# Optimization experiments

Hardware: AMD Instinct MI355X
Metric: run time of the kernel (lower is better)

The kernel has to match this reference:

```python
import jax, jax.numpy as jnp
import numpy as np

EPS = 1e-6
D = 1152          # hidden_size
NH_HEADS = 16     # num_attention_heads
HD = D // NH_HEADS
INTER = 4304      # intermediate_size
H4 = 4 * D        # 4608
I4 = 4 * INTER    # 17216
B, H, W = 8, 64, 64
WH, WW = 2, 2


def setup_inputs() -> dict:
    key = jax.random.key(0)
    ks = jax.random.split(key, 12)
    s = 0.02
    inp = {
        "hidden_states": jax.random.normal(ks[0], (B, H * W, D), jnp.float32),
        "tgt_sizes": jnp.full((B, 2), 64, dtype=jnp.int32),
        "attention_mask": jnp.zeros((B, 1, 1, H * W), jnp.float32),
        "ln1_g": jnp.ones((D,), jnp.float32),
        "ln1_b": jnp.zeros((D,), jnp.float32),
        "qkv_w": jax.random.normal(ks[1], (D, 3 * D), jnp.float32) * s,
        "qkv_b": jnp.zeros((3 * D,), jnp.float32),
        "out_w": jax.random.normal(ks[2], (D, D), jnp.float32) * s,
        "out_b": jnp.zeros((D,), jnp.float32),
        "pre_g": jnp.ones((H4,), jnp.float32),
        "pre_b": jnp.zeros((H4,), jnp.float32),
        "w1": jax.random.normal(ks[3], (H4, I4), jnp.float32) * s,
        "b1": jnp.zeros((I4,), jnp.float32),
        "w2": jax.random.normal(ks[4], (I4, D), jnp.float32) * s,
        "b2": jnp.zeros((D,), jnp.float32),
    }
    return inp


def _layernorm(x, g, b):
    m = x.mean(-1, keepdims=True)
    v = ((x - m) ** 2).mean(-1, keepdims=True)
    return (x - m) * jax.lax.rsqrt(v + EPS) * g + b


def _partition(x):
    # x: [B, H*W, D] -> windows [B, nh*nw, wh*ww, D]
    nh, nw = H // WH, W // WW
    x = x.reshape(B, nh, WH, nw, WW, D)
    x = x.transpose(0, 1, 3, 2, 4, 5)  # [B, nh, nw, wh, ww, D]
    return x.reshape(B, nh * nw, WH * WW, D)


def _unpartition(x):
    # windows [B, nh*nw, wh*ww, D] -> [B, H*W, D]
    nh, nw = H // WH, W // WW
    x = x.reshape(B, nh, nw, WH, WW, D)
    x = x.transpose(0, 1, 3, 2, 4, 5)  # [B, nh, wh, nw, ww, D]
    return x.reshape(B, H * W, D)


def reference(hidden_states, tgt_sizes, attention_mask, ln1_g, ln1_b,
              qkv_w, qkv_b, out_w, out_b, pre_g, pre_b, w1, b1, w2, b2):
    nh, nw = H // WH, W // WW
    nwin = nh * nw
    residual = hidden_states
    hs = _layernorm(hidden_states, ln1_g, ln1_b)

    # window self-attention over 4-token windows
    xw = _partition(hs).reshape(B * nwin, WH * WW, D)
    qkv = xw @ qkv_w + qkv_b                               # [N, 4, 3D]
    q, k, v = jnp.split(qkv, 3, axis=-1)
    q = q.reshape(-1, WH * WW, NH_HEADS, HD)
    k = k.reshape(-1, WH * WW, NH_HEADS, HD)
    v = v.reshape(-1, WH * WW, NH_HEADS, HD)
    scale = HD ** -0.5
    scores = jnp.einsum('nqhd,nkhd->nhqk', q, k) * scale
    probs = jax.nn.softmax(scores, axis=-1)
    o = jnp.einsum('nhqk,nkhd->nqhd', probs, v).reshape(-1, WH * WW, D)
    o = o @ out_w + out_b
    attn_out = _unpartition(o.reshape(B, nwin, WH * WW, D))
    hs = residual + attn_out                               # [B, H*W, D]

    # MLP downsample over 2x2 windows
    xw = _partition(hs)                                    # [B, nwin, 4, D]
    res = xw.mean(axis=2)                                  # [B, nwin, D]
    xf = xw.reshape(B, nwin, WH * WW * D)                  # [B, nwin, 4D]
    xf = _layernorm(xf, pre_g, pre_b)
    xf = jax.nn.gelu(xf @ w1 + b1, approximate=True)
    xf = xf @ w2 + b2
    new_hidden = xf + res                                  # [B, nwin, D]

    new_tgt_sizes = tgt_sizes // 2
    # all samples fully valid -> mask of zeros (no -inf positions)
    min_val = jnp.finfo(new_hidden.dtype).min
    valid = jnp.arange(nwin)[None, :] < (new_tgt_sizes[:, 0] * new_tgt_sizes[:, 1])[:, None]
    new_attention_mask = ((~valid).astype(new_hidden.dtype) * min_val)[:, None, None, :]
    return new_hidden, new_tgt_sizes, new_attention_mask
```

## Files before the change

kernel.cpp:

```cpp
#include <hip/hip_runtime.h>
#include <cstdint>
#include <cstddef>

#define DEV __device__ __forceinline__
typedef unsigned short u16;
typedef unsigned int u32;
typedef short bf16x8 __attribute__((ext_vector_type(8)));
typedef float f32x4 __attribute__((ext_vector_type(4)));

typedef __attribute__((address_space(1))) u32 GU32;
typedef __attribute__((address_space(3))) u32 LU32;

DEV float bf2f(u16 v){ u32 x = ((u32)v)<<16; float f; __builtin_memcpy(&f,&x,4); return f; }
DEV u16 f2bf(float f){ u32 x; __builtin_memcpy(&x,&f,4); return (u16)((x + 0x7fffu + ((x>>16)&1u)) >> 16); }

DEV int map_row(int r){
  int b = r>>12, rr = r&4095;
  int win = rr>>2, t = rr&3;
  int wy = win>>5, wx = win&31;
  int y = (wy<<1) + (t>>1), x = (wx<<1) + (t&1);
  return (b<<12) + (y<<6) + x;
}

DEV void gl_lds16(const void* g, void* l){
  __builtin_amdgcn_global_load_lds((const GU32*)g, (LU32*)l, 16, 0, 0);
}

DEV void block_red2(float& s, float& ss, float* red){
  #pragma unroll
  for (int o=32;o;o>>=1){ s += __shfl_down(s,o); ss += __shfl_down(ss,o); }
  const int wv = threadIdx.x>>6;
  if ((threadIdx.x&63)==0){ red[wv*2]=s; red[wv*2+1]=ss; }
  __syncthreads();
  s  = red[0]+red[2]+red[4]+red[6];
  ss = red[1]+red[3]+red[5]+red[7];
}

__launch_bounds__(256)
__global__ void tconv_k(const float* __restrict__ W, u16* __restrict__ WT, int K, int N){
  __shared__ float tl[64][65];
  const int n0 = blockIdx.x << 6, k0 = blockIdx.y << 6;
  const int tx = threadIdx.x & 63, ty = threadIdx.x >> 6;
  #pragma unroll
  for (int rr = 0; rr < 64; rr += 4)
    tl[rr+ty][tx] = W[(size_t)(k0+rr+ty)*N + (n0+tx)];
  __syncthreads();
  #pragma unroll
  for (int rr = 0; rr < 64; rr += 4)
    WT[(size_t)(n0+rr+ty)*K + (k0+tx)] = f2bf(tl[tx][rr+ty]);
}

__launch_bounds__(256)
__global__ void ln1_k(const float* __restrict__ X, const float* __restrict__ g,
                      const float* __restrict__ b, u16* __restrict__ Y){
  __shared__ float red[8];
  const int r = blockIdx.x;
  const float* xr = X + (size_t)map_row(r)*1152;
  const int tid = threadIdx.x;
  const bool has2 = tid < 32;
  float4 v0 = ((const float4*)xr)[tid];
  float4 v1 = {0,0,0,0};
  float s  = v0.x+v0.y+v0.z+v0.w;
  float ss = v0.x*v0.x+v0.y*v0.y+v0.z*v0.z+v0.w*v0.w;
  if (has2){
    v1 = ((const float4*)xr)[tid+256];
    s  += v1.x+v1.y+v1.z+v1.w;
    ss += v1.x*v1.x+v1.y*v1.y+v1.z*v1.z+v1.w*v1.w;
  }
  block_red2(s, ss, red);
  const float mean = s*(1.0f/1152.0f);
  const float rstd = rsqrtf(ss*(1.0f/1152.0f) - mean*mean + 1e-6f);
  u16* yr = Y + (size_t)r*1152;
  {
    float4 gg = ((const float4*)g)[tid];
    float4 bb = ((const float4*)b)[tid];
    ushort4 o;
    o.x = f2bf((v0.x-mean)*rstd*gg.x + bb.x);
    o.y = f2bf((v0.y-mean)*rstd*gg.y + bb.y);
    o.z = f2bf((v0.z-mean)*rstd*gg.z + bb.z);
    o.w = f2bf((v0.w-mean)*rstd*gg.w + bb.w);
    *(ushort4*)(yr + tid*4) = o;
  }
  if (has2){
    float4 gg = ((const float4*)g)[tid+256];
    float4 bb = ((const float4*)b)[tid+256];
    ushort4 o;
    o.x = f2bf((v1.x-mean)*rstd*gg.x + bb.x);
    o.y = f2bf((v1.y-mean)*rstd*gg.y + bb.y);
    o.z = f2bf((v1.z-mean)*rstd*gg.z + bb.z);
    o.w = f2bf((v1.w-mean)*rstd*gg.w + bb.w);
    *(ushort4*)(yr + (tid+256)*4) = o;
  }
}

#define BAR()  asm volatile("s_barrier" ::: "memory")
#define LGKM0() do{ asm volatile("s_waitcnt lgkmcnt(0)" ::: "memory"); \
                    __builtin_amdgcn_sched_barrier(0); }while(0)
#define VMW8() asm volatile("s_waitcnt vmcnt(8)" ::: "memory")
#define VMW6() asm volatile("s_waitcnt vmcnt(6)" ::: "memory")
#define VMW4() asm volatile("s_waitcnt vmcnt(4)" ::: "memory")
#define VMW0() asm volatile("s_waitcnt vmcnt(0)" ::: "memory")
#define WNONE() do{}while(0)

template<int EPI>
__launch_bounds__(512, 1)
__global__ void gemm8p_k(const u16* __restrict__ A, const u16* __restrict__ BT,
                         int M, int N, int K, int lda, int ldb,
                         void* __restrict__ C, int ldc,
                         const float* __restrict__ bias,
                         const float* __restrict__ aux,
                         int nTM, int nTN)
{
  __shared__ __align__(16) u16 LS[2][2][2][8192];
  const int tid = threadIdx.x;
  const int lane = tid & 63;
  const int wave = tid >> 6;
  const int wr = wave >> 2, wc = wave & 3;

  const int bid  = blockIdx.x;
  const int band = 16 * nTN;
  const int bb   = bid / band, rr_ = bid % band;
  int mcnt = nTM - (bb<<4); if (mcnt > 16) mcnt = 16;
  const int mt = (bb<<4) + rr_ % mcnt;
  const int nt = rr_ / mcnt;
  const int m0 = mt << 8, n0 = nt << 8;

  const int lr1 = tid >> 3, sl = tid & 7;
  const int x_  = sl ^ (lr1 & 7);
  const int grow = ((x_ >> 2) << 7) + lr1;
  const int q_   = x_ & 3;
  const u16* aS = A  + (size_t)(m0 + grow)*lda + q_*8;
  const u16* bS = BT + (size_t)(n0 + grow)*ldb + q_*8;
  const size_t aR64 = (size_t)64*lda, bR64 = (size_t)64*ldb;

  const int l15 = lane & 15, l7 = lane & 7, qh = lane >> 4;
  const int aOff = l15*64 + ((((wr<<2)|qh) ^ l7) << 3);
  const int bOff = ((wc&1)<<12) + l15*64 + (((((wc>>1)<<2)|qh) ^ l7) << 3);

  f32x4 acc[8][4] = {};
  bf16x8 af[4], bv[4];
  const int NT = K >> 6;

#define ST(op_, db_, kh_, t_) do{ \
    const u16* src__ = (op_ ? bS : aS) + (size_t)(t_)*64 + (kh_)*32; \
    u16* dst__ = &LS[(db_)][(op_)][(kh_)][tid*8]; \
    gl_lds16(src__, dst__); \
    gl_lds16(src__ + (op_ ? bR64 : aR64), dst__ + 4096); \
  }while(0)

#define READA(base_, mh_) do{ \
    const u16* ap__ = (base_) + aOff + ((mh_)?4096:0); \
    _Pragma("unroll") for (int i__=0;i__<4;i__++) af[i__] = *(const bf16x8*)(ap__ + i__*1024); \
  }while(0)

#define READB(base_) do{ \
    const u16* bp__ = (base_) + bOff; \
    _Pragma("unroll") for (int i__=0;i__<4;i__++) bv[i__] = *(const bf16x8*)(bp__ + i__*1024); \
  }while(0)

#define MFMA16(B_) do{ \
    __builtin_amdgcn_s_setprio(1); \
    _Pragma("unroll") for (int i__=0;i__<4;i__++) \
      _Pragma("unroll") for (int n__=0;n__<4;n__++) \
        acc[(B_)+i__][n__] = __builtin_amdgcn_mfma_f32_16x16x32_bf16(af[i__], bv[n__], acc[(B_)+i__][n__], 0,0,0); \
    __builtin_amdgcn_s_setprio(0); \
  }while(0)

#define GROUP(t_, SE12, SE3, Wp1, Wp3) do{ \
    const int cb__ = (t_) & 1; \
    const u16* rA0__ = &LS[cb__][0][0][0]; \
    const u16* rB0__ = &LS[cb__][1][0][0]; \
    const u16* rA1__ = &LS[cb__][0][1][0]; \
    const u16* rB1__ = &LS[cb__][1][1][0]; \
    READB(rB0__); READA(rA0__, 0); \
    BAR(); LGKM0(); MFMA16(0); \
    READA(rA0__, 1); if (SE12) ST(0, cb__^1, 1, (t_)+1); \
    Wp1(); BAR(); LGKM0(); MFMA16(4); \
    READB(rB1__); READA(rA1__, 0); if (SE12) ST(1, cb__^1, 1, (t_)+1); \
    BAR(); LGKM0(); MFMA16(0); \
    READA(rA1__, 1); if (SE3) { ST(0, cb__, 0, (t_)+2); ST(1, cb__, 0, (t_)+2); } \
    Wp3(); BAR(); LGKM0(); MFMA16(4); \
  }while(0)

  ST(0,0,0,0); ST(1,0,0,0); ST(0,0,1,0); ST(1,0,1,0); ST(0,1,0,1); ST(1,1,0,1);
  VMW8(); BAR();

  int t = 0;
  for (; t < NT-2; ++t) GROUP(t, 1, 1, VMW6, VMW8);
  GROUP(t, 1, 0, VMW6, VMW4); ++t;
  GROUP(t, 0, 0, VMW0, WNONE);

#undef GROUP
#undef MFMA16
#undef READB
#undef READA
#undef ST

  #pragma unroll
  for (int mi=0;mi<8;mi++){
    const int row = m0 + (wr<<7) + (mi<<4) + ((lane>>4)<<2);
    #pragma unroll
    for (int ni=0;ni<4;ni++){
      const int col = n0 + (wc<<6) + (ni<<4) + (lane&15);
      if (col < N){
        const float bvv = bias[col];
        #pragma unroll
        for (int r2=0;r2<4;r2++){
          const int rw = row + r2;
          float v = acc[mi][ni][r2] + bvv;
          if (EPI==0){
            ((u16*)C)[(size_t)rw*ldc + col] = f2bf(v);
          } else if (EPI==1){
            v += aux[(size_t)map_row(rw)*ldc + col];
            ((u16*)C)[(size_t)rw*ldc + col] = f2bf(v);
          } else if (EPI==2){
            const float x = v;
            const float c = 0.7978845608028654f*(x + 0.044715f*x*x*x);
            v = 0.5f*x*(1.0f + tanhf(c));
            ((u16*)C)[(size_t)rw*ldc + col] = f2bf(v);
          } else {
            v += aux[(size_t)rw*ldc + col];
            ((float*)C)[(size_t)rw*ldc + col] = v;
          }
        }
      }
    }
  }
}

__launch_bounds__(256)
__global__ void attn_k(const u16* __restrict__ QKV, u16* __restrict__ O){
  const int wave = threadIdx.x >> 6, lane = threadIdx.x & 63;
  const int wg = blockIdx.x*4 + wave;
  const int t = lane >> 4, h = lane & 15;
  const u16* base = QKV + (size_t)wg*4*3456;

  float q[72];
  {
    const u16* qp = base + t*3456 + h*72;
    #pragma unroll
    for (int i=0;i<9;i++){
      bf16x8 v = *(const bf16x8*)(qp + i*8);
      #pragma unroll
      for (int j=0;j<8;j++) q[i*8+j] = bf2f((u16)v[j]);
    }
  }
  float sc[4];
  #pragma unroll
  for (int tp=0;tp<4;tp++){
    const u16* kp = base + tp*3456 + 1152 + h*72;
    float a = 0.f;
    #pragma unroll
    for (int i=0;i<9;i++){
      bf16x8 v = *(const bf16x8*)(kp + i*8);
      #pragma unroll
      for (int j=0;j<8;j++) a += q[i*8+j]*bf2f((u16)v[j]);
    }
    sc[tp] = a * 0.11785113019775793f;
  }
  const float mx = fmaxf(fmaxf(sc[0],sc[1]), fmaxf(sc[2],sc[3]));
  float p[4]; float sum = 0.f;
  #pragma unroll
  for (int tp=0;tp<4;tp++){ p[tp] = __expf(sc[tp]-mx); sum += p[tp]; }
  const float inv = 1.0f/sum;
  float o[72];
  #pragma unroll
  for (int i=0;i<72;i++) o[i] = 0.f;
  #pragma unroll
  for (int tp=0;tp<4;tp++){
    const float w = p[tp]*inv;
    const u16* vp = base + tp*3456 + 2304 + h*72;
    #pragma unroll
    for (int i=0;i<9;i++){
      bf16x8 v = *(const bf16x8*)(vp + i*8);
      #pragma unroll
      for (int j=0;j<8;j++) o[i*8+j] += w*bf2f((u16)v[j]);
    }
  }
  u16* op = O + (size_t)(wg*4+t)*1152 + h*72;
  #pragma unroll
  for (int i=0;i<9;i++){
    bf16x8 sv;
    #pragma unroll
    for (int j=0;j<8;j++) sv[j] = (short)f2bf(o[i*8+j]);
    *(bf16x8*)(op + i*8) = sv;
  }
}

__launch_bounds__(256)
__global__ void ln2res_k(const u16* __restrict__ hs2, const float* __restrict__ g,
                         const float* __restrict__ b, u16* __restrict__ Y,
                         float* __restrict__ res){
  __shared__ float buf[4608];
  __shared__ float red[8];
  const int w = blockIdx.x;
  const u16* xr = hs2 + (size_t)w*4608;
  float s = 0.f, ss = 0.f;
  for (int i = threadIdx.x*8; i < 4608; i += 2048){
    bf16x8 v = *(const bf16x8*)(xr + i);
    #pragma unroll
    for (int j=0;j<8;j++){
      float f = bf2f((u16)v[j]);
      buf[i+j] = f; s += f; ss += f*f;
    }
  }
  block_red2(s, ss, red);
  const float mean = s*(1.0f/4608.0f);
  const float rstd = rsqrtf(ss*(1.0f/4608.0f) - mean*mean + 1e-6f);
  u16* yr = Y + (size_t)w*4608;
  for (int i = threadIdx.x*8; i < 4608; i += 2048){
    bf16x8 sv;
    #pragma unroll
    for (int j=0;j<8;j++)
      sv[j] = (short)f2bf((buf[i+j]-mean)*rstd*g[i+j] + b[i+j]);
    *(bf16x8*)(yr + i) = sv;
  }
  for (int d = threadIdx.x; d < 1152; d += 256)
    res[(size_t)w*1152 + d] = 0.25f*(buf[d]+buf[d+1152]+buf[d+2304]+buf[d+3456]);
}

__global__ void tail_k(const int* __restrict__ tgt, float* __restrict__ out){
  const int tid = blockIdx.x*blockDim.x + threadIdx.x;
  float* t_out = out + 9437184;
  float* m_out = t_out + 16;
  if (tid < 16) t_out[tid] = (float)(tgt[tid] / 2);
  for (int i = tid; i < 8192; i += 256*32){
    const int b = i >> 10, w = i & 1023;
    const int lim = (tgt[b*2]/2) * (tgt[b*2+1]/2);
    m_out[i] = (w < lim) ? 0.0f : -3.40282346638528859812e+38f;
  }
}

extern "C" void kernel_launch(void* const* d_in, const int* in_sizes, int n_in,
                              void* d_out, int out_size, void* d_ws, size_t ws_size,
                              hipStream_t stream){
  const float* hidden = (const float*)d_in[0];
  const int*   tgt    = (const int*)  d_in[1];
  const float* ln1_g  = (const float*)d_in[3];
  const float* ln1_b  = (const float*)d_in[4];
  const float* qkv_w  = (const float*)d_in[5];
  const float* qkv_b  = (const float*)d_in[6];
  const float* out_w  = (const float*)d_in[7];
  const float* out_b  = (const float*)d_in[8];
  const float* pre_g  = (const float*)d_in[9];
  const float* pre_b  = (const float*)d_in[10];
  const float* w1     = (const float*)d_in[11];
  const float* b1     = (const float*)d_in[12];
  const float* w2     = (const float*)d_in[13];
  const float* b2     = (const float*)d_in[14];
  float* out = (float*)d_out;

  char* p = (char*)d_ws;
  auto alloc = [&](size_t bytes)->void*{ void* r = p; p += (bytes + 255) & ~(size_t)255; return r; };
  u16* w1T = (u16*)alloc(17216ull*4608*2);
  u16* w2T = (u16*)alloc(1152ull*17216*2);
  u16* wqT = (u16*)alloc(3456ull*1152*2);
  u16* woT = (u16*)alloc(1152ull*1152*2);
  u16* Xln = (u16*)alloc(32768ull*1152*2);
  char* qr = (char*)alloc(32768ull*3456*2);
  u16*   QKV  = (u16*)qr;
  u16*   hs2  = (u16*)qr;
  float* res  = (float*)(qr + 75497472);
  u16*   xfln = (u16*)(qr + 150994944);
  size_t fixed = (size_t)(p - (char*)d_ws);
  size_t avail = ws_size > fixed ? ws_size - fixed : 0;
  long long crl = (long long)((avail / (17216ull*2)) & ~(size_t)255);
  int CR = (int)(crl > 8192 ? 8192 : crl);
  if (CR < 256) CR = 256;
  u16* h1 = (u16*)p;

  tconv_k<<<dim3(17216/64, 4608/64), 256, 0, stream>>>(w1, w1T, 4608, 17216);
  tconv_k<<<dim3(1152/64, 17216/64), 256, 0, stream>>>(w2, w2T, 17216, 1152);
  tconv_k<<<dim3(3456/64, 1152/64), 256, 0, stream>>>(qkv_w, wqT, 1152, 3456);
  tconv_k<<<dim3(1152/64, 1152/64), 256, 0, stream>>>(out_w, woT, 1152, 1152);
  ln1_k<<<32768, 256, 0, stream>>>(hidden, ln1_g, ln1_b, Xln);
  gemm8p_k<0><<<dim3(128*14), 512, 0, stream>>>(Xln, wqT, 32768, 3456, 1152, 1152, 1152,
                                                QKV, 3456, qkv_b, nullptr, 128, 14);
  attn_k<<<2048, 256, 0, stream>>>(QKV, Xln);
  gemm8p_k<1><<<dim3(128*5), 512, 0, stream>>>(Xln, woT, 32768, 1152, 1152, 1152, 1152,
                                               hs2, 1152, out_b, hidden, 128, 5);
  ln2res_k<<<8192, 256, 0, stream>>>(hs2, pre_g, pre_b, xfln, res);
  for (int r0 = 0; r0 < 8192; r0 += CR){
    const int m = (8192 - r0 < CR) ? (8192 - r0) : CR;
    gemm8p_k<2><<<dim3((m>>8)*68), 512, 0, stream>>>(xfln + (size_t)r0*4608, w1T,
                                                     m, 17216, 4608, 4608, 4608,
                                                     h1, 17216, b1, nullptr, m>>8, 68);
    gemm8p_k<3><<<dim3((m>>8)*5), 512, 0, stream>>>(h1, w2T,
                                                    m, 1152, 17216, 17216, 17216,
                                                    out + (size_t)r0*1152, 1152, b2,
                                                    res + (size_t)r0*1152, m>>8, 5);
  }
  tail_k<<<32, 256, 0, stream>>>(tgt, out);
}
```

Measured before the change: 2.411 ms.

## Load GEMM B operand directly from global into registers, stage only A in LDS

The GEMM kernel drops LDS staging for the weight (B) operand. Each wave now loads its B fragments straight from global memory into registers, while A is still double-buffered in LDS. The main loop is simplified to one barrier per K-tile, replacing the four-phase grouped schedule with its fine-grained waitcnts. This halves LDS traffic and footprint and cuts barriers, but B reads become uncoalesced 16-byte per-lane global loads with no cross-wave reuse, and the direct loads may expose global latency.

```diff
diff --git a/kernel.cpp b/kernel.cpp
--- a/kernel.cpp
+++ b/kernel.cpp
@@ -94,24 +94,18 @@
 }
 
 #define BAR()  asm volatile("s_barrier" ::: "memory")
-#define LGKM0() do{ asm volatile("s_waitcnt lgkmcnt(0)" ::: "memory"); \
-                    __builtin_amdgcn_sched_barrier(0); }while(0)
 #define VMW8() asm volatile("s_waitcnt vmcnt(8)" ::: "memory")
-#define VMW6() asm volatile("s_waitcnt vmcnt(6)" ::: "memory")
-#define VMW4() asm volatile("s_waitcnt vmcnt(4)" ::: "memory")
-#define VMW0() asm volatile("s_waitcnt vmcnt(0)" ::: "memory")
-#define WNONE() do{}while(0)
 
 template<int EPI>
 __launch_bounds__(512, 1)
-__global__ void gemm8p_k(const u16* __restrict__ A, const u16* __restrict__ BT,
+__global__ void gemmbr_k(const u16* __restrict__ A, const u16* __restrict__ BT,
                          int M, int N, int K, int lda, int ldb,
                          void* __restrict__ C, int ldc,
                          const float* __restrict__ bias,
                          const float* __restrict__ aux,
                          int nTM, int nTN)
 {
-  __shared__ __align__(16) u16 LS[2][2][2][8192];
+  __shared__ __align__(16) u16 LSA[2][2][8192];
   const int tid = threadIdx.x;
   const int lane = tid & 63;
   const int wave = tid >> 6;
@@ -129,72 +123,75 @@
   const int x_  = sl ^ (lr1 & 7);
   const int grow = ((x_ >> 2) << 7) + lr1;
   const int q_   = x_ & 3;
-  const u16* aS = A  + (size_t)(m0 + grow)*lda + q_*8;
-  const u16* bS = BT + (size_t)(n0 + grow)*ldb + q_*8;
-  const size_t aR64 = (size_t)64*lda, bR64 = (size_t)64*ldb;
+  const u16* aS = A + (size_t)(m0 + grow)*lda + q_*8;
+  const size_t aR64 = (size_t)64*lda;
 
   const int l15 = lane & 15, l7 = lane & 7, qh = lane >> 4;
   const int aOff = l15*64 + ((((wr<<2)|qh) ^ l7) << 3);
-  const int bOff = ((wc&1)<<12) + l15*64 + (((((wc>>1)<<2)|qh) ^ l7) << 3);
+
+  const u16* bP[4];
+  #pragma unroll
+  for (int ni=0;ni<4;ni++)
+    bP[ni] = BT + (size_t)(n0 + (wc<<6) + (ni<<4) + l15)*ldb + (qh<<3);
 
   f32x4 acc[8][4] = {};
-  bf16x8 af[4], bv[4];
+  bf16x8 af[8];
+  bf16x8 bB[4][2];
   const int NT = K >> 6;
 
-#define ST(op_, db_, kh_, t_) do{ \
-    const u16* src__ = (op_ ? bS : aS) + (size_t)(t_)*64 + (kh_)*32; \
-    u16* dst__ = &LS[(db_)][(op_)][(kh_)][tid*8]; \
-    gl_lds16(src__, dst__); \
-    gl_lds16(src__ + (op_ ? bR64 : aR64), dst__ + 4096); \
+#define STAGEA(slotW_, t_) do{ \
+    _Pragma("unroll") for (int kh__=0;kh__<2;kh__++){ \
+      const u16* src__ = aS + (size_t)(t_)*64 + kh__*32; \
+      u16* dst__ = (slotW_) + kh__*8192 + tid*8; \
+      gl_lds16(src__, dst__); \
+      gl_lds16(src__ + aR64, dst__ + 4096); \
+    } \
   }while(0)
 
-#define READA(base_, mh_) do{ \
-    const u16* ap__ = (base_) + aOff + ((mh_)?4096:0); \
-    _Pragma("unroll") for (int i__=0;i__<4;i__++) af[i__] = *(const bf16x8*)(ap__ + i__*1024); \
+#define DSA(slotR_, kh_) do{ \
+    const u16* ap__ = (slotR_) + (kh_)*8192 + aOff; \
+    _Pragma("unroll") for (int j__=0;j__<8;j__++) af[j__] = *(const bf16x8*)(ap__ + j__*1024); \
   }while(0)
 
-#define READB(base_) do{ \
-    const u16* bp__ = (base_) + bOff; \
-    _Pragma("unroll") for (int i__=0;i__<4;i__++) bv[i__] = *(const bf16x8*)(bp__ + i__*1024); \
+#define LOADB(t_) do{ \
+    _Pragma("unroll") for (int ni__=0;ni__<4;ni__++) \
+      _Pragma("unroll") for (int h__=0;h__<2;h__++) \
+        bB[ni__][h__] = *(const bf16x8*)(bP[ni__] + (size_t)(t_)*64 + h__*32); \
   }while(0)
 
-#define MFMA16(B_) do{ \
+#define MFMAH(h_) do{ \
     __builtin_amdgcn_s_setprio(1); \
-    _Pragma("unroll") for (int i__=0;i__<4;i__++) \
-      _Pragma("unroll") for (int n__=0;n__<4;n__++) \
-        acc[(B_)+i__][n__] = __builtin_amdgcn_mfma_f32_16x16x32_bf16(af[i__], bv[n__], acc[(B_)+i__][n__], 0,0,0); \
+    _Pragma("unroll") for (int mi__=0;mi__<8;mi__++) \
+      _Pragma("unroll") for (int ni__=0;ni__<4;ni__++) \
+        acc[mi__][ni__] = __builtin_amdgcn_mfma_f32_16x16x32_bf16(af[mi__], bB[ni__][h_], acc[mi__][ni__], 0,0,0); \
     __builtin_amdgcn_s_setprio(0); \
   }while(0)
 
-#define GROUP(t_, SE12, SE3, Wp1, Wp3) do{ \
-    const int cb__ = (t_) & 1; \
-    const u16* rA0__ = &LS[cb__][0][0][0]; \
-    const u16* rB0__ = &LS[cb__][1][0][0]; \
-    const u16* rA1__ = &LS[cb__][0][1][0]; \
-    const u16* rB1__ = &LS[cb__][1][1][0]; \
-    READB(rB0__); READA(rA0__, 0); \
-    BAR(); LGKM0(); MFMA16(0); \
-    READA(rA0__, 1); if (SE12) ST(0, cb__^1, 1, (t_)+1); \
-    Wp1(); BAR(); LGKM0(); MFMA16(4); \
-    READB(rB1__); READA(rA1__, 0); if (SE12) ST(1, cb__^1, 1, (t_)+1); \
-    BAR(); LGKM0(); MFMA16(0); \
-    READA(rA1__, 1); if (SE3) { ST(0, cb__, 0, (t_)+2); ST(1, cb__, 0, (t_)+2); } \
-    Wp3(); BAR(); LGKM0(); MFMA16(4); \
-  }while(0)
-
-  ST(0,0,0,0); ST(1,0,0,0); ST(0,0,1,0); ST(1,0,1,0); ST(0,1,0,1); ST(1,1,0,1);
+  STAGEA(&LSA[0][0][0], 0);
+  __builtin_amdgcn_sched_barrier(0);
+  LOADB(0);
   VMW8(); BAR();
 
-  int t = 0;
-  for (; t < NT-2; ++t) GROUP(t, 1, 1, VMW6, VMW8);
-  GROUP(t, 1, 0, VMW6, VMW4); ++t;
-  GROUP(t, 0, 0, VMW0, WNONE);
-
-#undef GROUP
-#undef MFMA16
-#undef READB
-#undef READA
-#undef ST
+  for (int t = 0; t < NT; ++t){
+    u16* slotR = &LSA[t&1][0][0];
+    u16* slotW = &LSA[(t+1)&1][0][0];
+    const bool SA = (t+1 < NT);
+    if (SA){ STAGEA(slotW, t+1); __builtin_amdgcn_sched_barrier(0); }
+    DSA(slotR, 0);
+    MFMAH(0);
+    DSA(slotR, 1);
+    MFMAH(1);
+    if (SA){
+      LOADB(t+1);
+      VMW8();
+      BAR();
+    }
+  }
+
+#undef MFMAH
+#undef LOADB
+#undef DSA
+#undef STAGEA
 
   #pragma unroll
   for (int mi=0;mi<8;mi++){
@@ -374,18 +371,18 @@
   tconv_k<<<dim3(3456/64, 1152/64), 256, 0, stream>>>(qkv_w, wqT, 1152, 3456);
   tconv_k<<<dim3(1152/64, 1152/64), 256, 0, stream>>>(out_w, woT, 1152, 1152);
   ln1_k<<<32768, 256, 0, stream>>>(hidden, ln1_g, ln1_b, Xln);
-  gemm8p_k<0><<<dim3(128*14), 512, 0, stream>>>(Xln, wqT, 32768, 3456, 1152, 1152, 1152,
+  gemmbr_k<0><<<dim3(128*14), 512, 0, stream>>>(Xln, wqT, 32768, 3456, 1152, 1152, 1152,
                                                 QKV, 3456, qkv_b, nullptr, 128, 14);
   attn_k<<<2048, 256, 0, stream>>>(QKV, Xln);
-  gemm8p_k<1><<<dim3(128*5), 512, 0, stream>>>(Xln, woT, 32768, 1152, 1152, 1152, 1152,
+  gemmbr_k<1><<<dim3(128*5), 512, 0, stream>>>(Xln, woT, 32768, 1152, 1152, 1152, 1152,
                                                hs2, 1152, out_b, hidden, 128, 5);
   ln2res_k<<<8192, 256, 0, stream>>>(hs2, pre_g, pre_b, xfln, res);
   for (int r0 = 0; r0 < 8192; r0 += CR){
     const int m = (8192 - r0 < CR) ? (8192 - r0) : CR;
-    gemm8p_k<2><<<dim3((m>>8)*68), 512, 0, stream>>>(xfln + (size_t)r0*4608, w1T,
+    gemmbr_k<2><<<dim3((m>>8)*68), 512, 0, stream>>>(xfln + (size_t)r0*4608, w1T,
                                                      m, 17216, 4608, 4608, 4608,
                                                      h1, 17216, b1, nullptr, m>>8, 68);
-    gemm8p_k<3><<<dim3((m>>8)*5), 512, 0, stream>>>(h1, w2T,
+    gemmbr_k<3><<<dim3((m>>8)*5), 512, 0, stream>>>(h1, w2T,
                                                     m, 1152, 17216, 17216, 17216,
                                                     out + (size_t)r0*1152, 1152, b2,
                                                     res + (size_t)r0*1152, m>>8, 5);
```

After: 3.698 ms, median of 2. +53.4%, slower.

## Split-K the down-projection GEMM and reduce partials in a finalize kernel

Applied to the files above, without the earlier changes.

Adds a K-split mode to the GEMM kernel, driven by blockIdx.y and a per-split tile count. Each split writes fp32 partial sums to a scratch buffer that reuses the xfln workspace. The second MLP GEMM now runs as two K-halves, which doubles the block count from 160 tiles. A new fin_k kernel then sums the two partials with the bias and residual. The intent is better CU occupancy for a GEMM whose output tile grid is small, at the cost of extra fp32 partial traffic and one more kernel launch. The path is used only when the workspace fits the full 8192-row chunk.

```diff
diff --git a/kernel.cpp b/kernel.cpp
--- a/kernel.cpp
+++ b/kernel.cpp
@@ -109,13 +109,17 @@
                          void* __restrict__ C, int ldc,
                          const float* __restrict__ bias,
                          const float* __restrict__ aux,
-                         int nTM, int nTN)
+                         int nTM, int nTN, int ktile0)
 {
   __shared__ __align__(16) u16 LS[2][2][2][8192];
   const int tid = threadIdx.x;
   const int lane = tid & 63;
   const int wave = tid >> 6;
   const int wr = wave >> 2, wc = wave & 3;
+
+  const int ky  = (int)blockIdx.y;
+  const int kt0 = ky * ktile0;
+  const int NT  = (ky == (int)gridDim.y - 1) ? (K>>6) - kt0 : ktile0;
 
   const int bid  = blockIdx.x;
   const int band = 16 * nTN;
@@ -129,8 +133,8 @@
   const int x_  = sl ^ (lr1 & 7);
   const int grow = ((x_ >> 2) << 7) + lr1;
   const int q_   = x_ & 3;
-  const u16* aS = A  + (size_t)(m0 + grow)*lda + q_*8;
-  const u16* bS = BT + (size_t)(n0 + grow)*ldb + q_*8;
+  const u16* aS = A  + (size_t)(m0 + grow)*lda + (size_t)kt0*64 + q_*8;
+  const u16* bS = BT + (size_t)(n0 + grow)*ldb + (size_t)kt0*64 + q_*8;
   const size_t aR64 = (size_t)64*lda, bR64 = (size_t)64*ldb;
 
   const int l15 = lane & 15, l7 = lane & 7, qh = lane >> 4;
@@ -139,7 +143,6 @@
 
   f32x4 acc[8][4] = {};
   bf16x8 af[4], bv[4];
-  const int NT = K >> 6;
 
 #define ST(op_, db_, kh_, t_) do{ \
     const u16* src__ = (op_ ? bS : aS) + (size_t)(t_)*64 + (kh_)*32; \
@@ -196,6 +199,8 @@
 #undef READA
 #undef ST
 
+  float* Cp = (EPI==4) ? ((float*)C + (size_t)ky*M*ldc) : nullptr;
+
   #pragma unroll
   for (int mi=0;mi<8;mi++){
     const int row = m0 + (wr<<7) + (mi<<4) + ((lane>>4)<<2);
@@ -203,7 +208,7 @@
     for (int ni=0;ni<4;ni++){
       const int col = n0 + (wc<<6) + (ni<<4) + (lane&15);
       if (col < N){
-        const float bvv = bias[col];
+        const float bvv = (EPI==4) ? 0.f : bias[col];
         #pragma unroll
         for (int r2=0;r2<4;r2++){
           const int rw = row + r2;
@@ -218,13 +223,34 @@
             const float c = 0.7978845608028654f*(x + 0.044715f*x*x*x);
             v = 0.5f*x*(1.0f + tanhf(c));
             ((u16*)C)[(size_t)rw*ldc + col] = f2bf(v);
-          } else {
+          } else if (EPI==3){
             v += aux[(size_t)rw*ldc + col];
             ((float*)C)[(size_t)rw*ldc + col] = v;
+          } else {
+            Cp[(size_t)rw*ldc + col] = v;
           }
         }
       }
     }
+  }
+}
+
+__launch_bounds__(256)
+__global__ void fin_k(const float* __restrict__ P, const float* __restrict__ res,
+                      const float* __restrict__ bias, float* __restrict__ out){
+  const int total4 = 8192*288;
+  for (int i = blockIdx.x*256 + threadIdx.x; i < total4; i += 2048*256){
+    const int c4 = i % 288;
+    float4 a = ((const float4*)P)[i];
+    float4 b = ((const float4*)P)[i + total4];
+    float4 r = ((const float4*)res)[i];
+    float4 g = ((const float4*)bias)[c4];
+    float4 o;
+    o.x = a.x + b.x + r.x + g.x;
+    o.y = a.y + b.y + r.y + g.y;
+    o.z = a.z + b.z + r.z + g.z;
+    o.w = a.w + b.w + r.w + g.w;
+    ((float4*)out)[i] = o;
   }
 }
 
@@ -362,6 +388,7 @@
   u16*   hs2  = (u16*)qr;
   float* res  = (float*)(qr + 75497472);
   u16*   xfln = (u16*)(qr + 150994944);
+  float* P    = (float*)(qr + 150994944);
   size_t fixed = (size_t)(p - (char*)d_ws);
   size_t avail = ws_size > fixed ? ws_size - fixed : 0;
   long long crl = (long long)((avail / (17216ull*2)) & ~(size_t)255);
@@ -375,20 +402,28 @@
   tconv_k<<<dim3(1152/64, 1152/64), 256, 0, stream>>>(out_w, woT, 1152, 1152);
   ln1_k<<<32768, 256, 0, stream>>>(hidden, ln1_g, ln1_b, Xln);
   gemm8p_k<0><<<dim3(128*14), 512, 0, stream>>>(Xln, wqT, 32768, 3456, 1152, 1152, 1152,
-                                                QKV, 3456, qkv_b, nullptr, 128, 14);
+                                                QKV, 3456, qkv_b, nullptr, 128, 14, 1152>>6);
   attn_k<<<2048, 256, 0, stream>>>(QKV, Xln);
   gemm8p_k<1><<<dim3(128*5), 512, 0, stream>>>(Xln, woT, 32768, 1152, 1152, 1152, 1152,
-                                               hs2, 1152, out_b, hidden, 128, 5);
+                                               hs2, 1152, out_b, hidden, 128, 5, 1152>>6);
   ln2res_k<<<8192, 256, 0, stream>>>(hs2, pre_g, pre_b, xfln, res);
-  for (int r0 = 0; r0 < 8192; r0 += CR){
-    const int m = (8192 - r0 < CR) ? (8192 - r0) : CR;
-    gemm8p_k<2><<<dim3((m>>8)*68), 512, 0, stream>>>(xfln + (size_t)r0*4608, w1T,
-                                                     m, 17216, 4608, 4608, 4608,
-                                                     h1, 17216, b1, nullptr, m>>8, 68);
-    gemm8p_k<3><<<dim3((m>>8)*5), 512, 0, stream>>>(h1, w2T,
-                                                    m, 1152, 17216, 17216, 17216,
-                                                    out + (size_t)r0*1152, 1152, b2,
-                                                    res + (size_t)r0*1152, m>>8, 5);
+  if (CR >= 8192){
+    gemm8p_k<2><<<dim3(32*68), 512, 0, stream>>>(xfln, w1T, 8192, 17216, 4608, 4608, 4608,
+                                                 h1, 17216, b1, nullptr, 32, 68, 4608>>6);
+    gemm8p_k<4><<<dim3(32*5, 2), 512, 0, stream>>>(h1, w2T, 8192, 1152, 17216, 17216, 17216,
+                                                   P, 1152, b2, nullptr, 32, 5, 134);
+    fin_k<<<2048, 256, 0, stream>>>(P, res, b2, out);
+  } else {
+    for (int r0 = 0; r0 < 8192; r0 += CR){
+      const int m = (8192 - r0 < CR) ? (8192 - r0) : CR;
+      gemm8p_k<2><<<dim3((m>>8)*68), 512, 0, stream>>>(xfln + (size_t)r0*4608, w1T,
+                                                       m, 17216, 4608, 4608, 4608,
+                                                       h1, 17216, b1, nullptr, m>>8, 68, 4608>>6);
+      gemm8p_k<3><<<dim3((m>>8)*5), 512, 0, stream>>>(h1, w2T,
+                                                      m, 1152, 17216, 17216, 17216,
+                                                      out + (size_t)r0*1152, 1152, b2,
+                                                      res + (size_t)r0*1152, m>>8, 5, 17216>>6);
+    }
   }
   tail_k<<<32, 256, 0, stream>>>(tgt, out);
 }
```

New measurement: 2.437 ms. Within noise of the previous version (+1.1%).
